# Optimization experiments

Measured on AMD Instinct MI355X. Metric: run time of the kernel, lower is better.

The kernel has to match this reference:

```python
import jax, jax.numpy as jnp
import numpy as np

IMAGE_MAX_DIM = 1024
POOL = 7
NUM_CLASSES = 81
N_ROIS = 2000
BN_EPS = 1e-3


def _make_boxes(key, n):
    k1, k2, k3, k4 = jax.random.split(key, 4)
    cx = jax.random.uniform(k1, (n,), minval=0.0, maxval=IMAGE_MAX_DIM)
    cy = jax.random.uniform(k2, (n,), minval=0.0, maxval=IMAGE_MAX_DIM)
    w = jax.random.uniform(k3, (n,), minval=16.0, maxval=512.0)
    h = jax.random.uniform(k4, (n,), minval=16.0, maxval=512.0)
    x1 = jnp.clip(cx - w / 2, 0.0, IMAGE_MAX_DIM - 2.0)
    y1 = jnp.clip(cy - h / 2, 0.0, IMAGE_MAX_DIM - 2.0)
    x2 = jnp.clip(cx + w / 2, x1 + 1.0, IMAGE_MAX_DIM)
    y2 = jnp.clip(cy + h / 2, y1 + 1.0, IMAGE_MAX_DIM)
    return jnp.stack([x1, y1, x2, y2], axis=-1)[None]  # [1, n, 4]


def setup_inputs() -> dict:
    key = jax.random.key(0)
    ks = jax.random.split(key, 16)
    d = {
        'p2': jax.random.normal(ks[0], (1, 256, 256, 256), jnp.float32),
        'p3': jax.random.normal(ks[1], (1, 256, 128, 128), jnp.float32),
        'p4': jax.random.normal(ks[2], (1, 256, 64, 64), jnp.float32),
        'p5': jax.random.normal(ks[3], (1, 256, 32, 32), jnp.float32),
        'rpn_rois': _make_boxes(ks[4], N_ROIS),
        'conv1_w': jax.random.normal(ks[5], (1024, 256, POOL, POOL), jnp.float32) * 0.02,
        'conv1_b': jnp.zeros((1024,), jnp.float32),
        'bn1_g': jnp.ones((1024,), jnp.float32),
        'bn1_b': jnp.zeros((1024,), jnp.float32),
        'bn1_m': jnp.zeros((1024,), jnp.float32),
        'bn1_v': jnp.ones((1024,), jnp.float32),
        'conv2_w': jax.random.normal(ks[6], (1024, 1024), jnp.float32) * 0.02,
        'conv2_b': jnp.zeros((1024,), jnp.float32),
        'bn2_g': jnp.ones((1024,), jnp.float32),
        'bn2_b': jnp.zeros((1024,), jnp.float32),
        'bn2_m': jnp.zeros((1024,), jnp.float32),
        'bn2_v': jnp.ones((1024,), jnp.float32),
        'logits_w': jax.random.normal(ks[7], (NUM_CLASSES, 1024), jnp.float32) * 0.02,
        'logits_b': jnp.zeros((NUM_CLASSES,), jnp.float32),
        'bbox_w': jax.random.normal(ks[8], (NUM_CLASSES * 4, 1024), jnp.float32) * 0.02,
        'bbox_b': jnp.zeros((NUM_CLASSES * 4,), jnp.float32),
    }
    return d


def _crop_resize(fmap, boxes):
    """TF-style crop_and_resize, bilinear. fmap [C,H,W]; boxes [N,4] = (y1,x1,y2,x2) normalized."""
    C, H, W = fmap.shape
    dt = fmap.dtype
    y1, x1, y2, x2 = boxes[:, 0], boxes[:, 1], boxes[:, 2], boxes[:, 3]
    t = (jnp.arange(POOL, dtype=dt) / (POOL - 1))  # [P]
    ys = y1[:, None] * (H - 1) + t[None, :] * ((y2 - y1) * (H - 1))[:, None]  # [N,P]
    xs = x1[:, None] * (W - 1) + t[None, :] * ((x2 - x1) * (W - 1))[:, None]  # [N,P]
    y0 = jnp.floor(ys)
    x0 = jnp.floor(xs)
    ly = (ys - y0)[None, :, :, None]  # [1,N,P,1]
    lx = (xs - x0)[None, :, None, :]  # [1,N,1,P]
    y0i = jnp.clip(y0.astype(jnp.int32), 0, H - 1)
    y1i = jnp.clip(y0i + 1, 0, H - 1)
    x0i = jnp.clip(x0.astype(jnp.int32), 0, W - 1)
    x1i = jnp.clip(x0i + 1, 0, W - 1)

    def g(yi, xi):  # -> [C,N,P,P]
        return fmap[:, yi[:, :, None], xi[:, None, :]]

    out = (g(y0i, x0i) * (1 - ly) * (1 - lx) + g(y0i, x1i) * (1 - ly) * lx
           + g(y1i, x0i) * ly * (1 - lx) + g(y1i, x1i) * ly * lx)
    return jnp.transpose(out, (1, 0, 2, 3))  # [N,C,P,P]


def _forward(p2, p3, p4, p5, rpn_rois, conv1_w, conv1_b, bn1_g, bn1_b, bn1_m, bn1_v,
             conv2_w, conv2_b, bn2_g, bn2_b, bn2_m, bn2_v, logits_w, logits_b, bbox_w, bbox_b):
    rois = rpn_rois.reshape(-1, 4)  # [N,4] (x1,y1,x2,y2) in pixels
    x1, y1, x2, y2 = rois[:, 0], rois[:, 1], rois[:, 2], rois[:, 3]
    # level = clamp(round(log2(sqrt(area)/224)) + 4, 2, 5)
    roi_level = jnp.clip(jnp.round(jnp.log2(jnp.sqrt((y2 - y1) * (x2 - x1)) / 224.0)) + 4.0, 2.0, 5.0)
    boxes_n = (rois / float(IMAGE_MAX_DIM))[:, [1, 0, 3, 2]]  # (y1,x1,y2,x2) normalized

    pooled = jnp.zeros((rois.shape[0], 256, POOL, POOL), rois.dtype)
    for lvl, fmap in zip(range(2, 6), [p2, p3, p4, p5]):
        crops = _crop_resize(fmap[0], boxes_n)  # [N,256,P,P]
        mask = (roi_level == float(lvl))[:, None, None, None]
        pooled = pooled + jnp.where(mask, crops, 0.0)

    # conv1: 7x7 valid conv over [N,256,7,7] -> [N,1024]
    h = jnp.einsum('nchw,ochw->no', pooled, conv1_w) + conv1_b
    h = (h - bn1_m) * jax.lax.rsqrt(bn1_v + BN_EPS) * bn1_g + bn1_b
    h = jax.nn.relu(h)
    # conv2: 1x1 conv == matmul
    h = h @ conv2_w.T + conv2_b
    h = (h - bn2_m) * jax.lax.rsqrt(bn2_v + BN_EPS) * bn2_g + bn2_b
    shared = jax.nn.relu(h)  # [N,1024]

    logits = shared @ logits_w.T + logits_b
    probs = jax.nn.softmax(logits, axis=-1)
    bbox = shared @ bbox_w.T + bbox_b
    return (logits.reshape(1, N_ROIS, NUM_CLASSES),
            probs.reshape(1, N_ROIS, NUM_CLASSES),
            bbox.reshape(1, N_ROIS, NUM_CLASSES, 4))


def reference(p2, p3, p4, p5, rpn_rois, conv1_w, conv1_b, bn1_g, bn1_b, bn1_m, bn1_v,
              conv2_w, conv2_b, bn2_g, bn2_b, bn2_m, bn2_v, logits_w, logits_b, bbox_w, bbox_b):
    return _forward(p2, p3, p4, p5, rpn_rois, conv1_w, conv1_b, bn1_g, bn1_b, bn1_m, bn1_v,
                    conv2_w, conv2_b, bn2_g, bn2_b, bn2_m, bn2_v, logits_w, logits_b, bbox_w, bbox_b)
```

## Files before the change

### kernel.cpp

```cpp
#include <hip/hip_runtime.h>
#include <stdint.h>

#define NROI 2000
#define MPAD 2048
#define KP   12544
#define N1   1024
#define NCLS 81
#define NBOX 324
#define N3   405
#define N3P  448
#define BN_EPS 0.001f
#define KSPLIT 8

typedef __attribute__((ext_vector_type(8))) short bf16x8;
typedef __attribute__((ext_vector_type(4))) float f32x4;
typedef __attribute__((ext_vector_type(8))) unsigned short u16x8;

__device__ inline unsigned short f2bf(float f) {
  union { float f; unsigned u; } v; v.f = f;
  unsigned r = v.u + 0x7fffu + ((v.u >> 16) & 1u);
  return (unsigned short)(r >> 16);
}

__device__ inline float bf2f(unsigned short h) {
  union { unsigned u; float f; } v; v.u = (unsigned)h << 16; return v.f;
}

__device__ inline void gld16(const unsigned short* g, unsigned short* l) {
  __builtin_amdgcn_global_load_lds(
      (const __attribute__((address_space(1))) void*)g,
      (__attribute__((address_space(3))) void*)l, 16, 0, 0);
}

__device__ __forceinline__ void kslice(int kz, int& off, int& len) {
  if (kz < 4) { off = kz * 1536; len = 1536; }
  else        { off = 6144 + (kz - 4) * 1600; len = 1600; }
}

__global__ __launch_bounds__(256) void front(
    const float* __restrict__ c1w, const float* __restrict__ c2w,
    const float* __restrict__ lw, const float* __restrict__ bw,
    const float* c1b, const float* g1, const float* b1, const float* m1, const float* v1,
    const float* c2b, const float* g2, const float* b2, const float* m2, const float* v2,
    const float* lb, const float* bb,
    const float* __restrict__ p2, const float* __restrict__ p3,
    const float* __restrict__ p4, const float* __restrict__ p5,
    unsigned short* __restrict__ w1p, unsigned short* __restrict__ w2b,
    unsigned short* __restrict__ w3b,
    unsigned short* __restrict__ f2t, unsigned short* __restrict__ f3t,
    unsigned short* __restrict__ f4t, unsigned short* __restrict__ f5t,
    float* s1, float* t1, float* s2, float* t2, float* b3) {
  __shared__ unsigned short srep[KP];
  int b = blockIdx.x;
  int t = threadIdx.x;
  if (b < 1360) {
    int bb2 = b;
    const float* src;
    unsigned short* dst;
    int HW;
    if (bb2 < 1024)      { src = p2; dst = f2t; HW = 65536; }
    else if (bb2 < 1280) { bb2 -= 1024; src = p3; dst = f3t; HW = 16384; }
    else if (bb2 < 1344) { bb2 -= 1280; src = p4; dst = f4t; HW = 4096; }
    else                 { bb2 -= 1344; src = p5; dst = f5t; HW = 1024; }
    int p0 = bb2 * 64;
    int lane = t & 63, w = t >> 6;
    int pq = (lane & 15) * 4;
    int cg = (lane >> 4) * 8;
#pragma unroll
    for (int it = 0; it < 2; ++it) {
      int c = w * 64 + it * 32 + cg;
      const float* sp = src + (size_t)c * HW + p0 + pq;
      float4 v[8];
#pragma unroll
      for (int k = 0; k < 8; ++k)
        v[k] = *(const float4*)(sp + (size_t)k * HW);
      unsigned short* dp = dst + (size_t)(p0 + pq) * 256 + c;
      u16x8 o0, o1, o2, o3;
#pragma unroll
      for (int k = 0; k < 8; ++k) {
        o0[k] = f2bf(v[k].x);
        o1[k] = f2bf(v[k].y);
        o2[k] = f2bf(v[k].z);
        o3[k] = f2bf(v[k].w);
      }
      *(u16x8*)(dp)       = o0;
      *(u16x8*)(dp + 256) = o1;
      *(u16x8*)(dp + 512) = o2;
      *(u16x8*)(dp + 768) = o3;
    }
  } else if (b < 2384) {
    int o = b - 1360;
    const float4* src = (const float4*)(c1w + (size_t)o * KP);
    for (int k = t; k < 3136; k += 256) {
      float4 v = src[k];
      ushort4 q;
      q.x = f2bf(v.x); q.y = f2bf(v.y); q.z = f2bf(v.z); q.w = f2bf(v.w);
      *(ushort4*)&srep[k * 4] = q;
    }
    __syncthreads();
    unsigned short* dst = w1p + (size_t)o * KP;
    int lane = t & 63, w = t >> 6;
    int c4 = lane * 4;
    for (int j = w; j < 49; j += 4) {
      ushort4 q;
      q.x = srep[(c4 + 0) * 49 + j];
      q.y = srep[(c4 + 1) * 49 + j];
      q.z = srep[(c4 + 2) * 49 + j];
      q.w = srep[(c4 + 3) * 49 + j];
      *(ushort4*)(dst + j * 256 + c4) = q;
    }
  } else if (b < 3408) {
    int j4 = (b - 2384) * 256 + t;
    float4 v = ((const float4*)c2w)[j4];
    ushort4 q;
    q.x = f2bf(v.x); q.y = f2bf(v.y); q.z = f2bf(v.z); q.w = f2bf(v.w);
    *(ushort4*)(w2b + (size_t)j4 * 4) = q;
  } else if (b < 3856) {
    int row = b - 3408;
    int k = t * 4;
    float4 v = {0.f, 0.f, 0.f, 0.f};
    if (row < NCLS)      v = *(const float4*)(lw + (size_t)row * 1024 + k);
    else if (row < N3)   v = *(const float4*)(bw + (size_t)(row - NCLS) * 1024 + k);
    ushort4 q;
    q.x = f2bf(v.x); q.y = f2bf(v.y); q.z = f2bf(v.z); q.w = f2bf(v.w);
    *(ushort4*)(w3b + (size_t)row * 1024 + k) = q;
  } else {
    for (int i = t; i < 1024; i += 256) {
      float sc = g1[i] * rsqrtf(v1[i] + BN_EPS);
      s1[i] = sc;
      t1[i] = (c1b[i] - m1[i]) * sc + b1[i];
      float ss = g2[i] * rsqrtf(v2[i] + BN_EPS);
      s2[i] = ss;
      t2[i] = (c2b[i] - m2[i]) * ss + b2[i];
    }
    for (int i = t; i < N3P; i += 256)
      b3[i] = (i < NCLS) ? lb[i] : (i < N3 ? bb[i - NCLS] : 0.0f);
  }
}

__global__ __launch_bounds__(256) void roi_align2(
    const unsigned short* __restrict__ f2t, const unsigned short* __restrict__ f3t,
    const unsigned short* __restrict__ f4t, const unsigned short* __restrict__ f5t,
    const float* __restrict__ rois, unsigned short* __restrict__ pooled) {
  int n = blockIdx.x;
  int t = threadIdx.x;
  int lane = t & 63, w = t >> 6;
  int c0 = lane * 4;
  unsigned short* out = pooled + (size_t)n * KP;
  if (n >= NROI) {
    for (int p = w; p < 49; p += 4)
      *(ushort4*)(out + p * 256 + c0) = make_ushort4(0, 0, 0, 0);
    return;
  }
  float x1 = rois[n * 4 + 0], y1 = rois[n * 4 + 1];
  float x2 = rois[n * 4 + 2], y2 = rois[n * 4 + 3];
  float area = (y2 - y1) * (x2 - x1);
  float lvl_f = rintf(log2f(sqrtf(area) / 224.0f)) + 4.0f;
  lvl_f = fminf(fmaxf(lvl_f, 2.0f), 5.0f);
  int lvl = (int)lvl_f;
  const unsigned short* f;
  int H;
  if (lvl == 2)      { f = f2t; H = 256; }
  else if (lvl == 3) { f = f3t; H = 128; }
  else if (lvl == 4) { f = f4t; H = 64;  }
  else               { f = f5t; H = 32;  }
  int W = H;
  const float inv = 1.0f / 1024.0f;
  float yn1 = y1 * inv, xn1 = x1 * inv, yn2 = y2 * inv, xn2 = x2 * inv;
  float hs = (yn2 - yn1) * (H - 1);
  float ws = (xn2 - xn1) * (W - 1);
  float yb = yn1 * (H - 1);
  float xb = xn1 * (W - 1);

  for (int p = w; p < 49; p += 4) {
    int py = p / 7, px = p - py * 7;
    float ysv = yb + ((float)py / 6.0f) * hs;
    float xsv = xb + ((float)px / 6.0f) * ws;
    float y0f = floorf(ysv), x0f = floorf(xsv);
    float ly = ysv - y0f, lx = xsv - x0f;
    int y0 = min(max((int)y0f, 0), H - 1);
    int y1i = min(y0 + 1, H - 1);
    int x0 = min(max((int)x0f, 0), W - 1);
    int x1i = min(x0 + 1, W - 1);
    ushort4 v00 = *(const ushort4*)(f + ((size_t)y0 * W + x0) * 256 + c0);
    ushort4 v01 = *(const ushort4*)(f + ((size_t)y0 * W + x1i) * 256 + c0);
    ushort4 v10 = *(const ushort4*)(f + ((size_t)y1i * W + x0) * 256 + c0);
    ushort4 v11 = *(const ushort4*)(f + ((size_t)y1i * W + x1i) * 256 + c0);
    ushort4 o;
    {
      float a = bf2f(v00.x), bq = bf2f(v01.x), cq = bf2f(v10.x), d = bf2f(v11.x);
      float top = a + lx * (bq - a), bot = cq + lx * (d - cq);
      o.x = f2bf(top + ly * (bot - top));
    }
    {
      float a = bf2f(v00.y), bq = bf2f(v01.y), cq = bf2f(v10.y), d = bf2f(v11.y);
      float top = a + lx * (bq - a), bot = cq + lx * (d - cq);
      o.y = f2bf(top + ly * (bot - top));
    }
    {
      float a = bf2f(v00.z), bq = bf2f(v01.z), cq = bf2f(v10.z), d = bf2f(v11.z);
      float top = a + lx * (bq - a), bot = cq + lx * (d - cq);
      o.z = f2bf(top + ly * (bot - top));
    }
    {
      float a = bf2f(v00.w), bq = bf2f(v01.w), cq = bf2f(v10.w), d = bf2f(v11.w);
      float top = a + lx * (bq - a), bot = cq + lx * (d - cq);
      o.w = f2bf(top + ly * (bot - top));
    }
    *(ushort4*)(out + p * 256 + c0) = o;
  }
}

__global__ __launch_bounds__(512, 2) void gemm1_sk2(
    const unsigned short* __restrict__ A, const unsigned short* __restrict__ B,
    unsigned short* __restrict__ part) {
  __shared__ unsigned short AsF[4 * 8192];
  __shared__ unsigned short BsF[4 * 8192];
  int bid = blockIdx.x;
  int kz = bid & 7;
  int u = bid >> 3;
  int bn0 = (u & 3) * 256;
  int bm0 = (u >> 2) * 256;
  int koff, klen;
  kslice(kz, koff, klen);
  int nt = klen >> 6;

  int t = threadIdx.x;
  int lane = t & 63, w = t >> 6;
  int wr = w >> 2, wc = w & 3;
  int ln = lane & 15, q = lane >> 4;

  int clog = (lane & 3) ^ ((lane >> 3) & 3);
  int l4 = lane >> 2;
  const unsigned short* gA0 = A + (size_t)(bm0 + w * 32 + l4) * KP + koff + clog * 8;
  const unsigned short* gA1 = gA0 + (size_t)16 * KP;
  const unsigned short* gB0 = B + (size_t)(bn0 + w * 32 + l4) * KP + koff + clog * 8;
  const unsigned short* gB1 = gB0 + (size_t)16 * KP;
  int dc0 = (w * 128 + lane) * 8;
  int dc1 = dc0 + 64 * 8;

  int rxor = (q ^ ((ln >> 1) & 3)) * 8;
  int rdA = (wr * 128 + ln) * 32 + rxor;
  int rdB = (wc * 64 + ln) * 32 + rxor;

  f32x4 acc[8][4] = {};

#pragma unroll
  for (int kk = 0; kk < 2; ++kk) {
    int src = kk * 32;
    int db = kk * 8192;
    gld16(gA0 + src, AsF + db + dc0);
    gld16(gA1 + src, AsF + db + dc1);
    gld16(gB0 + src, BsF + db + dc0);
    gld16(gB1 + src, BsF + db + dc1);
  }
  asm volatile("s_waitcnt vmcnt(4)" ::: "memory");
  __builtin_amdgcn_s_barrier();
  asm volatile("" ::: "memory");

  for (int tt = 0; tt < nt; ++tt) {
    int slot = tt & 1;
    int nslot = slot ^ 1;
    int knext = (tt + 1 < nt) ? (tt + 1) * 64 : 0;
#pragma unroll
    for (int kk = 0; kk < 2; ++kk) {
      int rb = (slot * 2 + kk) * 8192;
      bf16x8 af[8], bfr[4];
#pragma unroll
      for (int mi = 0; mi < 8; ++mi)
        af[mi] = *(const bf16x8*)&AsF[rb + rdA + mi * 512];
#pragma unroll
      for (int nj = 0; nj < 4; ++nj)
        bfr[nj] = *(const bf16x8*)&BsF[rb + rdB + nj * 512];

      int src = knext + kk * 32;
      int db = (nslot * 2 + kk) * 8192;
      gld16(gA0 + src, AsF + db + dc0);
      gld16(gA1 + src, AsF + db + dc1);
      gld16(gB0 + src, BsF + db + dc0);
      gld16(gB1 + src, BsF + db + dc1);

      asm volatile("s_waitcnt vmcnt(4)" ::: "memory");
      __builtin_amdgcn_s_barrier();
      asm volatile("" ::: "memory");

      __builtin_amdgcn_s_setprio(1);
#pragma unroll
      for (int mi = 0; mi < 8; ++mi)
#pragma unroll
        for (int nj = 0; nj < 4; ++nj)
          acc[mi][nj] = __builtin_amdgcn_mfma_f32_16x16x32_bf16(
              af[mi], bfr[nj], acc[mi][nj], 0, 0, 0);
      __builtin_amdgcn_s_setprio(0);

      asm volatile("" ::: "memory");
      __builtin_amdgcn_s_barrier();
      asm volatile("" ::: "memory");
    }
  }

  unsigned short* po = part + (size_t)kz * MPAD * N1;
#pragma unroll
  for (int mi = 0; mi < 8; ++mi) {
    int m = bm0 + wr * 128 + mi * 16 + q * 4;
#pragma unroll
    for (int nj = 0; nj < 4; ++nj) {
      int n = bn0 + wc * 64 + nj * 16 + ln;
#pragma unroll
      for (int r = 0; r < 4; ++r)
        po[(size_t)(m + r) * N1 + n] = f2bf(acc[mi][nj][r]);
    }
  }
}

__global__ void reduce_sk(const unsigned short* __restrict__ part,
                          const float* __restrict__ sc, const float* __restrict__ sh,
                          unsigned short* __restrict__ outb) {
  const size_t P = (size_t)MPAD * N1;
  int m = blockIdx.x;
  int t = threadIdx.x;
  float4 v = {0.f, 0.f, 0.f, 0.f};
#pragma unroll
  for (int kz = 0; kz < KSPLIT; ++kz) {
    ushort4 u = *(const ushort4*)(part + kz * P + (size_t)m * N1 + t * 4);
    v.x += bf2f(u.x); v.y += bf2f(u.y); v.z += bf2f(u.z); v.w += bf2f(u.w);
  }
  int n0 = t * 4;
  ushort4 o;
  if (m < NROI) {
    o.x = f2bf(fmaxf(v.x * sc[n0 + 0] + sh[n0 + 0], 0.0f));
    o.y = f2bf(fmaxf(v.y * sc[n0 + 1] + sh[n0 + 1], 0.0f));
    o.z = f2bf(fmaxf(v.z * sc[n0 + 2] + sh[n0 + 2], 0.0f));
    o.w = f2bf(fmaxf(v.w * sc[n0 + 3] + sh[n0 + 3], 0.0f));
  } else {
    o = make_ushort4(0, 0, 0, 0);
  }
  *(ushort4*)(outb + (size_t)m * N1 + n0) = o;
}

template <int MODE>
__global__ __launch_bounds__(256) void gemm_bt(
    const unsigned short* __restrict__ A, const unsigned short* __restrict__ B,
    int M, int N, int K,
    const float* __restrict__ sc, const float* __restrict__ sh,
    unsigned short* __restrict__ outb, float* __restrict__ outf,
    int validM, int ldo) {
  __shared__ unsigned short As[64 * 64];
  __shared__ unsigned short Bs[64 * 64];
  int bm0 = blockIdx.y * 64;
  int bn0 = blockIdx.x * 64;
  int t = threadIdx.x;
  int lane = t & 63, w = t >> 6;
  int wm = (w & 1) * 32, wn = (w >> 1) * 32;
  int ln = lane & 15, q = lane >> 4;

  int r8 = t >> 3, j8 = t & 7;
  int sj = j8 ^ (r8 & 7);
  const unsigned short* ga = A + (size_t)(bm0 + r8) * K + sj * 8;
  const unsigned short* gb = B + (size_t)(bn0 + r8) * K + sj * 8;
  unsigned short* la = &As[t * 8];
  unsigned short* lb = &Bs[t * 8];
  int e = ln & 7;

  f32x4 acc00 = {0.f, 0.f, 0.f, 0.f}, acc01 = {0.f, 0.f, 0.f, 0.f};
  f32x4 acc10 = {0.f, 0.f, 0.f, 0.f}, acc11 = {0.f, 0.f, 0.f, 0.f};

  for (int k0 = 0; k0 < K; k0 += 64) {
    gld16(ga + k0, la);
    gld16(ga + k0 + (size_t)32 * K, la + 2048);
    gld16(gb + k0, lb);
    gld16(gb + k0 + (size_t)32 * K, lb + 2048);
    __syncthreads();
#pragma unroll
    for (int h = 0; h < 2; ++h) {
      int slot = ((h * 4 + q) ^ e) * 8;
      bf16x8 a0 = *(const bf16x8*)&As[(wm + ln) * 64 + slot];
      bf16x8 a1 = *(const bf16x8*)&As[(wm + 16 + ln) * 64 + slot];
      bf16x8 b0 = *(const bf16x8*)&Bs[(wn + ln) * 64 + slot];
      bf16x8 b1 = *(const bf16x8*)&Bs[(wn + 16 + ln) * 64 + slot];
      acc00 = __builtin_amdgcn_mfma_f32_16x16x32_bf16(a0, b0, acc00, 0, 0, 0);
      acc01 = __builtin_amdgcn_mfma_f32_16x16x32_bf16(a0, b1, acc01, 0, 0, 0);
      acc10 = __builtin_amdgcn_mfma_f32_16x16x32_bf16(a1, b0, acc10, 0, 0, 0);
      acc11 = __builtin_amdgcn_mfma_f32_16x16x32_bf16(a1, b1, acc11, 0, 0, 0);
    }
    __syncthreads();
  }

  f32x4 accs[2][2] = {{acc00, acc01}, {acc10, acc11}};
#pragma unroll
  for (int i = 0; i < 2; ++i)
#pragma unroll
    for (int j = 0; j < 2; ++j)
#pragma unroll
      for (int r = 0; r < 4; ++r) {
        int m = bm0 + wm + i * 16 + q * 4 + r;
        int n = bn0 + wn + j * 16 + ln;
        float v = accs[i][j][r];
        if (MODE == 1) {
          float o = fmaxf(v * sc[n] + sh[n], 0.0f);
          outb[(size_t)m * ldo + n] = (m < validM) ? f2bf(o) : (unsigned short)0;
        } else {
          outf[(size_t)m * ldo + n] = v + sh[n];
        }
      }
}

__global__ void head(const float* __restrict__ fc3, float* __restrict__ out) {
  int r = blockIdx.x;
  int t = threadIdx.x;
  const float* row = fc3 + (size_t)r * N3P;
  float v0 = (t < NCLS) ? row[t] : -INFINITY;
  float v1 = (t + 64 < NCLS) ? row[t + 64] : -INFINITY;
  float m = fmaxf(v0, v1);
#pragma unroll
  for (int o = 32; o > 0; o >>= 1) m = fmaxf(m, __shfl_xor(m, o, 64));
  float e0 = (t < NCLS) ? expf(v0 - m) : 0.0f;
  float e1 = (t + 64 < NCLS) ? expf(v1 - m) : 0.0f;
  float s = e0 + e1;
#pragma unroll
  for (int o = 32; o > 0; o >>= 1) s += __shfl_xor(s, o, 64);
  float invs = 1.0f / s;
  float* ol = out + (size_t)r * NCLS;
  float* op = out + 162000 + (size_t)r * NCLS;
  float* ob = out + 324000 + (size_t)r * NBOX;
  if (t < NCLS) { ol[t] = v0; op[t] = e0 * invs; }
  if (t + 64 < NCLS) { ol[t + 64] = v1; op[t + 64] = e1 * invs; }
  for (int j = t; j < NBOX; j += 64) ob[j] = row[NCLS + j];
}

extern "C" void kernel_launch(void* const* d_in, const int* in_sizes, int n_in,
                              void* d_out, int out_size, void* d_ws, size_t ws_size,
                              hipStream_t stream) {
  const float* p2  = (const float*)d_in[0];
  const float* p3  = (const float*)d_in[1];
  const float* p4  = (const float*)d_in[2];
  const float* p5  = (const float*)d_in[3];
  const float* roi = (const float*)d_in[4];
  const float* c1w = (const float*)d_in[5];
  const float* c1b = (const float*)d_in[6];
  const float* g1  = (const float*)d_in[7];
  const float* b1  = (const float*)d_in[8];
  const float* m1  = (const float*)d_in[9];
  const float* v1  = (const float*)d_in[10];
  const float* c2w = (const float*)d_in[11];
  const float* c2b = (const float*)d_in[12];
  const float* g2  = (const float*)d_in[13];
  const float* b2  = (const float*)d_in[14];
  const float* m2  = (const float*)d_in[15];
  const float* v2  = (const float*)d_in[16];
  const float* lw  = (const float*)d_in[17];
  const float* lb  = (const float*)d_in[18];
  const float* bw  = (const float*)d_in[19];
  const float* bb  = (const float*)d_in[20];
  float* out = (float*)d_out;

  char* ws = (char*)d_ws;
  size_t off = 0;
  auto alloc = [&](size_t bytes) {
    void* p = ws + off;
    off = (off + bytes + 255) & ~(size_t)255;
    return p;
  };
  unsigned short* pooled = (unsigned short*)alloc((size_t)MPAD * KP * 2);
  unsigned short* w1p    = (unsigned short*)alloc((size_t)N1 * KP * 2);
  unsigned short* w2b    = (unsigned short*)alloc((size_t)N1 * N1 * 2);
  unsigned short* w3b    = (unsigned short*)alloc((size_t)N3P * N1 * 2);
  unsigned short* a2     = (unsigned short*)alloc((size_t)MPAD * N1 * 2);
  unsigned short* shd    = (unsigned short*)alloc((size_t)MPAD * N1 * 2);
  float* fc3 = (float*)alloc((size_t)MPAD * N3P * 4);
  char* ub = (char*)alloc((size_t)48 * 1024 * 1024);
  unsigned short* f2t = (unsigned short*)ub;
  unsigned short* f3t = (unsigned short*)(ub + 33554432);
  unsigned short* f4t = (unsigned short*)(ub + 33554432 + 8388608);
  unsigned short* f5t = (unsigned short*)(ub + 33554432 + 8388608 + 2097152);
  unsigned short* part = (unsigned short*)ub;
  float* s1  = (float*)alloc(1024 * 4);
  float* t1  = (float*)alloc(1024 * 4);
  float* s2  = (float*)alloc(1024 * 4);
  float* t2  = (float*)alloc(1024 * 4);
  float* b3  = (float*)alloc(N3P * 4);

  front<<<3857, 256, 0, stream>>>(c1w, c2w, lw, bw,
                                  c1b, g1, b1, m1, v1, c2b, g2, b2, m2, v2,
                                  lb, bb, p2, p3, p4, p5,
                                  w1p, w2b, w3b, f2t, f3t, f4t, f5t,
                                  s1, t1, s2, t2, b3);

  roi_align2<<<MPAD, 256, 0, stream>>>(f2t, f3t, f4t, f5t, roi, pooled);

  gemm1_sk2<<<256, 512, 0, stream>>>(pooled, w1p, part);
  reduce_sk<<<MPAD, 256, 0, stream>>>(part, s1, t1, a2);

  gemm_bt<1><<<dim3(N1 / 64, MPAD / 64), 256, 0, stream>>>(
      a2, w2b, MPAD, N1, N1, s2, t2, shd, nullptr, NROI, N1);
  gemm_bt<2><<<dim3(N3P / 64, MPAD / 64), 256, 0, stream>>>(
      shd, w3b, MPAD, N3P, N1, nullptr, b3, nullptr, fc3, NROI, N3P);

  head<<<NROI, 64, 0, stream>>>(fc3, out);
}
```

Measured before the change: 312.5 us.

## Move weight conversion into roi_align launch and split conv1 weight repack

After: 315.4 us. About the same (+0.9%).

```diff
diff --git a/kernel.cpp b/kernel.cpp
--- a/kernel.cpp
+++ b/kernel.cpp
@@ -37,86 +37,160 @@
   else        { off = 6144 + (kz - 4) * 1600; len = 1600; }
 }
 
-__global__ __launch_bounds__(256) void front(
+__global__ __launch_bounds__(256) void front_t(
+    const float* __restrict__ p2, const float* __restrict__ p3,
+    const float* __restrict__ p4, const float* __restrict__ p5,
+    unsigned short* __restrict__ f2t, unsigned short* __restrict__ f3t,
+    unsigned short* __restrict__ f4t, unsigned short* __restrict__ f5t) {
+  int bb2 = blockIdx.x;
+  int t = threadIdx.x;
+  const float* src;
+  unsigned short* dst;
+  int HW;
+  if (bb2 < 1024)      { src = p2; dst = f2t; HW = 65536; }
+  else if (bb2 < 1280) { bb2 -= 1024; src = p3; dst = f3t; HW = 16384; }
+  else if (bb2 < 1344) { bb2 -= 1280; src = p4; dst = f4t; HW = 4096; }
+  else                 { bb2 -= 1344; src = p5; dst = f5t; HW = 1024; }
+  int p0 = bb2 * 64;
+  int lane = t & 63, w = t >> 6;
+  int pq = (lane & 15) * 4;
+  int cg = (lane >> 4) * 8;
+#pragma unroll
+  for (int it = 0; it < 2; ++it) {
+    int c = w * 64 + it * 32 + cg;
+    const float* sp = src + (size_t)c * HW + p0 + pq;
+    float4 v[8];
+#pragma unroll
+    for (int k = 0; k < 8; ++k)
+      v[k] = *(const float4*)(sp + (size_t)k * HW);
+    unsigned short* dp = dst + (size_t)(p0 + pq) * 256 + c;
+    u16x8 o0, o1, o2, o3;
+#pragma unroll
+    for (int k = 0; k < 8; ++k) {
+      o0[k] = f2bf(v[k].x);
+      o1[k] = f2bf(v[k].y);
+      o2[k] = f2bf(v[k].z);
+      o3[k] = f2bf(v[k].w);
+    }
+    *(u16x8*)(dp)       = o0;
+    *(u16x8*)(dp + 256) = o1;
+    *(u16x8*)(dp + 512) = o2;
+    *(u16x8*)(dp + 768) = o3;
+  }
+}
+
+__global__ __launch_bounds__(256) void roi_prep(
+    const unsigned short* __restrict__ f2t, const unsigned short* __restrict__ f3t,
+    const unsigned short* __restrict__ f4t, const unsigned short* __restrict__ f5t,
+    const float* __restrict__ rois, unsigned short* __restrict__ pooled,
     const float* __restrict__ c1w, const float* __restrict__ c2w,
     const float* __restrict__ lw, const float* __restrict__ bw,
     const float* c1b, const float* g1, const float* b1, const float* m1, const float* v1,
     const float* c2b, const float* g2, const float* b2, const float* m2, const float* v2,
     const float* lb, const float* bb,
-    const float* __restrict__ p2, const float* __restrict__ p3,
-    const float* __restrict__ p4, const float* __restrict__ p5,
     unsigned short* __restrict__ w1p, unsigned short* __restrict__ w2b,
     unsigned short* __restrict__ w3b,
-    unsigned short* __restrict__ f2t, unsigned short* __restrict__ f3t,
-    unsigned short* __restrict__ f4t, unsigned short* __restrict__ f5t,
     float* s1, float* t1, float* s2, float* t2, float* b3) {
-  __shared__ unsigned short srep[KP];
+  __shared__ unsigned short srep[6272];
   int b = blockIdx.x;
   int t = threadIdx.x;
-  if (b < 1360) {
-    int bb2 = b;
-    const float* src;
-    unsigned short* dst;
-    int HW;
-    if (bb2 < 1024)      { src = p2; dst = f2t; HW = 65536; }
-    else if (bb2 < 1280) { bb2 -= 1024; src = p3; dst = f3t; HW = 16384; }
-    else if (bb2 < 1344) { bb2 -= 1280; src = p4; dst = f4t; HW = 4096; }
-    else                 { bb2 -= 1344; src = p5; dst = f5t; HW = 1024; }
-    int p0 = bb2 * 64;
+  if (b < 2048) {
+    int n = b;
     int lane = t & 63, w = t >> 6;
-    int pq = (lane & 15) * 4;
-    int cg = (lane >> 4) * 8;
-#pragma unroll
-    for (int it = 0; it < 2; ++it) {
-      int c = w * 64 + it * 32 + cg;
-      const float* sp = src + (size_t)c * HW + p0 + pq;
-      float4 v[8];
-#pragma unroll
-      for (int k = 0; k < 8; ++k)
-        v[k] = *(const float4*)(sp + (size_t)k * HW);
-      unsigned short* dp = dst + (size_t)(p0 + pq) * 256 + c;
-      u16x8 o0, o1, o2, o3;
-#pragma unroll
-      for (int k = 0; k < 8; ++k) {
-        o0[k] = f2bf(v[k].x);
-        o1[k] = f2bf(v[k].y);
-        o2[k] = f2bf(v[k].z);
-        o3[k] = f2bf(v[k].w);
+    int c0 = lane * 4;
+    unsigned short* out = pooled + (size_t)n * KP;
+    if (n >= NROI) {
+      for (int p = w; p < 49; p += 4)
+        *(ushort4*)(out + p * 256 + c0) = make_ushort4(0, 0, 0, 0);
+      return;
+    }
+    float x1 = rois[n * 4 + 0], y1 = rois[n * 4 + 1];
+    float x2 = rois[n * 4 + 2], y2 = rois[n * 4 + 3];
+    float area = (y2 - y1) * (x2 - x1);
+    float lvl_f = rintf(log2f(sqrtf(area) / 224.0f)) + 4.0f;
+    lvl_f = fminf(fmaxf(lvl_f, 2.0f), 5.0f);
+    int lvl = (int)lvl_f;
+    const unsigned short* f;
+    int H;
+    if (lvl == 2)      { f = f2t; H = 256; }
+    else if (lvl == 3) { f = f3t; H = 128; }
+    else if (lvl == 4) { f = f4t; H = 64;  }
+    else               { f = f5t; H = 32;  }
+    int W = H;
+    const float inv = 1.0f / 1024.0f;
+    float yn1 = y1 * inv, xn1 = x1 * inv, yn2 = y2 * inv, xn2 = x2 * inv;
+    float hs = (yn2 - yn1) * (H - 1);
+    float ws = (xn2 - xn1) * (W - 1);
+    float yb = yn1 * (H - 1);
+    float xb = xn1 * (W - 1);
+
+    for (int p = w; p < 49; p += 4) {
+      int py = p / 7, px = p - py * 7;
+      float ysv = yb + ((float)py / 6.0f) * hs;
+      float xsv = xb + ((float)px / 6.0f) * ws;
+      float y0f = floorf(ysv), x0f = floorf(xsv);
+      float ly = ysv - y0f, lx = xsv - x0f;
+      int y0 = min(max((int)y0f, 0), H - 1);
+      int y1i = min(y0 + 1, H - 1);
+      int x0 = min(max((int)x0f, 0), W - 1);
+      int x1i = min(x0 + 1, W - 1);
+      ushort4 v00 = *(const ushort4*)(f + ((size_t)y0 * W + x0) * 256 + c0);
+      ushort4 v01 = *(const ushort4*)(f + ((size_t)y0 * W + x1i) * 256 + c0);
+      ushort4 v10 = *(const ushort4*)(f + ((size_t)y1i * W + x0) * 256 + c0);
+      ushort4 v11 = *(const ushort4*)(f + ((size_t)y1i * W + x1i) * 256 + c0);
+      ushort4 o;
+      {
+        float a = bf2f(v00.x), bq = bf2f(v01.x), cq = bf2f(v10.x), d = bf2f(v11.x);
+        float top = a + lx * (bq - a), bot = cq + lx * (d - cq);
+        o.x = f2bf(top + ly * (bot - top));
       }
-      *(u16x8*)(dp)       = o0;
-      *(u16x8*)(dp + 256) = o1;
-      *(u16x8*)(dp + 512) = o2;
-      *(u16x8*)(dp + 768) = o3;
-    }
-  } else if (b < 2384) {
-    int o = b - 1360;
-    const float4* src = (const float4*)(c1w + (size_t)o * KP);
-    for (int k = t; k < 3136; k += 256) {
+      {
+        float a = bf2f(v00.y), bq = bf2f(v01.y), cq = bf2f(v10.y), d = bf2f(v11.y);
+        float top = a + lx * (bq - a), bot = cq + lx * (d - cq);
+        o.y = f2bf(top + ly * (bot - top));
+      }
+      {
+        float a = bf2f(v00.z), bq = bf2f(v01.z), cq = bf2f(v10.z), d = bf2f(v11.z);
+        float top = a + lx * (bq - a), bot = cq + lx * (d - cq);
+        o.z = f2bf(top + ly * (bot - top));
+      }
+      {
+        float a = bf2f(v00.w), bq = bf2f(v01.w), cq = bf2f(v10.w), d = bf2f(v11.w);
+        float top = a + lx * (bq - a), bot = cq + lx * (d - cq);
+        o.w = f2bf(top + ly * (bot - top));
+      }
+      *(ushort4*)(out + p * 256 + c0) = o;
+    }
+  } else if (b < 4096) {
+    int idx = b - 2048;
+    int o = idx >> 1, h = idx & 1;
+    const float4* src = (const float4*)(c1w + (size_t)o * KP + h * 6272);
+    for (int k = t; k < 1568; k += 256) {
       float4 v = src[k];
       ushort4 q;
       q.x = f2bf(v.x); q.y = f2bf(v.y); q.z = f2bf(v.z); q.w = f2bf(v.w);
       *(ushort4*)&srep[k * 4] = q;
     }
     __syncthreads();
-    unsigned short* dst = w1p + (size_t)o * KP;
-    int lane = t & 63, w = t >> 6;
-    int c4 = lane * 4;
-    for (int j = w; j < 49; j += 4) {
+    unsigned short* dst = w1p + (size_t)o * KP + h * 128;
+    int ch4 = (t & 31) * 4;
+    int jw = t >> 5;
+    for (int j = jw; j < 49; j += 8) {
       ushort4 q;
-      q.x = srep[(c4 + 0) * 49 + j];
-      q.y = srep[(c4 + 1) * 49 + j];
-      q.z = srep[(c4 + 2) * 49 + j];
-      q.w = srep[(c4 + 3) * 49 + j];
-      *(ushort4*)(dst + j * 256 + c4) = q;
-    }
-  } else if (b < 3408) {
-    int j4 = (b - 2384) * 256 + t;
+      q.x = srep[(ch4 + 0) * 49 + j];
+      q.y = srep[(ch4 + 1) * 49 + j];
+      q.z = srep[(ch4 + 2) * 49 + j];
+      q.w = srep[(ch4 + 3) * 49 + j];
+      *(ushort4*)(dst + j * 256 + ch4) = q;
+    }
+  } else if (b < 5120) {
+    int j4 = (b - 4096) * 256 + t;
     float4 v = ((const float4*)c2w)[j4];
     ushort4 q;
     q.x = f2bf(v.x); q.y = f2bf(v.y); q.z = f2bf(v.z); q.w = f2bf(v.w);
     *(ushort4*)(w2b + (size_t)j4 * 4) = q;
-  } else if (b < 3856) {
-    int row = b - 3408;
+  } else if (b < 5568) {
+    int row = b - 5120;
     int k = t * 4;
     float4 v = {0.f, 0.f, 0.f, 0.f};
     if (row < NCLS)      v = *(const float4*)(lw + (size_t)row * 1024 + k);
@@ -135,79 +209,6 @@
     }
     for (int i = t; i < N3P; i += 256)
       b3[i] = (i < NCLS) ? lb[i] : (i < N3 ? bb[i - NCLS] : 0.0f);
-  }
-}
-
-__global__ __launch_bounds__(256) void roi_align2(
-    const unsigned short* __restrict__ f2t, const unsigned short* __restrict__ f3t,
-    const unsigned short* __restrict__ f4t, const unsigned short* __restrict__ f5t,
-    const float* __restrict__ rois, unsigned short* __restrict__ pooled) {
-  int n = blockIdx.x;
-  int t = threadIdx.x;
-  int lane = t & 63, w = t >> 6;
-  int c0 = lane * 4;
-  unsigned short* out = pooled + (size_t)n * KP;
-  if (n >= NROI) {
-    for (int p = w; p < 49; p += 4)
-      *(ushort4*)(out + p * 256 + c0) = make_ushort4(0, 0, 0, 0);
-    return;
-  }
-  float x1 = rois[n * 4 + 0], y1 = rois[n * 4 + 1];
-  float x2 = rois[n * 4 + 2], y2 = rois[n * 4 + 3];
-  float area = (y2 - y1) * (x2 - x1);
-  float lvl_f = rintf(log2f(sqrtf(area) / 224.0f)) + 4.0f;
-  lvl_f = fminf(fmaxf(lvl_f, 2.0f), 5.0f);
-  int lvl = (int)lvl_f;
-  const unsigned short* f;
-  int H;
-  if (lvl == 2)      { f = f2t; H = 256; }
-  else if (lvl == 3) { f = f3t; H = 128; }
-  else if (lvl == 4) { f = f4t; H = 64;  }
-  else               { f = f5t; H = 32;  }
-  int W = H;
-  const float inv = 1.0f / 1024.0f;
-  float yn1 = y1 * inv, xn1 = x1 * inv, yn2 = y2 * inv, xn2 = x2 * inv;
-  float hs = (yn2 - yn1) * (H - 1);
-  float ws = (xn2 - xn1) * (W - 1);
-  float yb = yn1 * (H - 1);
-  float xb = xn1 * (W - 1);
-
-  for (int p = w; p < 49; p += 4) {
-    int py = p / 7, px = p - py * 7;
-    float ysv = yb + ((float)py / 6.0f) * hs;
-    float xsv = xb + ((float)px / 6.0f) * ws;
-    float y0f = floorf(ysv), x0f = floorf(xsv);
-    float ly = ysv - y0f, lx = xsv - x0f;
-    int y0 = min(max((int)y0f, 0), H - 1);
-    int y1i = min(y0 + 1, H - 1);
-    int x0 = min(max((int)x0f, 0), W - 1);
-    int x1i = min(x0 + 1, W - 1);
-    ushort4 v00 = *(const ushort4*)(f + ((size_t)y0 * W + x0) * 256 + c0);
-    ushort4 v01 = *(const ushort4*)(f + ((size_t)y0 * W + x1i) * 256 + c0);
-    ushort4 v10 = *(const ushort4*)(f + ((size_t)y1i * W + x0) * 256 + c0);
-    ushort4 v11 = *(const ushort4*)(f + ((size_t)y1i * W + x1i) * 256 + c0);
-    ushort4 o;
-    {
-      float a = bf2f(v00.x), bq = bf2f(v01.x), cq = bf2f(v10.x), d = bf2f(v11.x);
-      float top = a + lx * (bq - a), bot = cq + lx * (d - cq);
-      o.x = f2bf(top + ly * (bot - top));
-    }
-    {
-      float a = bf2f(v00.y), bq = bf2f(v01.y), cq = bf2f(v10.y), d = bf2f(v11.y);
-      float top = a + lx * (bq - a), bot = cq + lx * (d - cq);
-      o.y = f2bf(top + ly * (bot - top));
-    }
-    {
-      float a = bf2f(v00.z), bq = bf2f(v01.z), cq = bf2f(v10.z), d = bf2f(v11.z);
-      float top = a + lx * (bq - a), bot = cq + lx * (d - cq);
-      o.z = f2bf(top + ly * (bot - top));
-    }
-    {
-      float a = bf2f(v00.w), bq = bf2f(v01.w), cq = bf2f(v10.w), d = bf2f(v11.w);
-      float top = a + lx * (bq - a), bot = cq + lx * (d - cq);
-      o.w = f2bf(top + ly * (bot - top));
-    }
-    *(ushort4*)(out + p * 256 + c0) = o;
   }
 }
 
@@ -480,13 +481,13 @@
   float* t2  = (float*)alloc(1024 * 4);
   float* b3  = (float*)alloc(N3P * 4);
 
-  front<<<3857, 256, 0, stream>>>(c1w, c2w, lw, bw,
-                                  c1b, g1, b1, m1, v1, c2b, g2, b2, m2, v2,
-                                  lb, bb, p2, p3, p4, p5,
-                                  w1p, w2b, w3b, f2t, f3t, f4t, f5t,
-                                  s1, t1, s2, t2, b3);
-
-  roi_align2<<<MPAD, 256, 0, stream>>>(f2t, f3t, f4t, f5t, roi, pooled);
+  front_t<<<1360, 256, 0, stream>>>(p2, p3, p4, p5, f2t, f3t, f4t, f5t);
+
+  roi_prep<<<5569, 256, 0, stream>>>(f2t, f3t, f4t, f5t, roi, pooled,
+                                     c1w, c2w, lw, bw,
+                                     c1b, g1, b1, m1, v1, c2b, g2, b2, m2, v2,
+                                     lb, bb,
+                                     w1p, w2b, w3b, s1, t1, s2, t2, b3);
 
   gemm1_sk2<<<256, 512, 0, stream>>>(pooled, w1p, part);
   reduce_sk<<<MPAD, 256, 0, stream>>>(part, s1, t1, a2);
```
